# Performance work log

Hardware: AMD Instinct MI355X
Metric: run time of the kernel (lower is better)

Reference implementation:

```python
import jax, jax.numpy as jnp
import numpy as np

LOCAL_REGION = 16
GRANULARITY = 2048
INIT_RATIO = 8
EXPAND_RATIO = 2
C = 128
N_LAYERS = 5


def setup_inputs() -> dict:
    key = jax.random.key(0)
    ks = jax.random.split(key, 20)
    g = lambda k, s: jax.random.normal(k, s, dtype=jnp.float32) * 0.05
    z = lambda n: jnp.zeros((n,), jnp.float32)
    return {
        "batch_x": jax.random.normal(ks[0], (1, 16384, 4), dtype=jnp.float32),
        # PT: attr embedding (in_channel=1 -> 128), positional MLP (3->128->128)
        "attr_w": g(ks[1], (1, C)), "attr_b": z(C),
        "pos_w1": g(ks[2], (3, C)), "pos_b1": z(C),
        "pos_w2": g(ks[3], (C, C)), "pos_b2": z(C),
        # 5 self-attention layers over the K-neighborhood
        "wq": g(ks[4], (N_LAYERS, C, C)),
        "wk": g(ks[5], (N_LAYERS, C, C)),
        "wv": g(ks[6], (N_LAYERS, C, C)),
        "wout": g(ks[7], (C, C)), "bout": z(C),
        # mu/sigma head: 128 -> 64 -> 16 -> 2
        "ms_w1": g(ks[8], (C, 64)), "ms_b1": z(64),
        "ms_w2": g(ks[9], (64, 16)), "ms_b2": z(16),
        "ms_w3": g(ks[10], (16, 2)), "ms_b3": z(2),
    }


def _window_schedule(N):
    base = min(N // INIT_RATIO, GRANULARITY)
    win = base
    sched = []
    cursor = base
    while cursor < N:
        win = min(win * EXPAND_RATIO, GRANULARITY)
        sched.append((cursor, min(win, N - cursor)))
        cursor += win
    return sched


def _forward(batch_x, attr_w, attr_b, pos_w1, pos_b1, pos_w2, pos_b2,
             wq, wk, wv, wout, bout, ms_w1, ms_b1, ms_w2, ms_b2, ms_w3, ms_b3):
    B, N, _ = batch_x.shape
    total_bits = jnp.float32(0.0)
    for cur, w in _window_schedule(N):
        context = batch_x[:, :cur, :]
        target = batch_x[:, cur:cur + w, :]
        tg, ta = target[..., :3], target[..., 3:]    # [B,M,3], [B,M,1]
        cg, ca = context[..., :3], context[..., 3:]  # [B,Nc,3], [B,Nc,1]
        # knn_points: brute-force squared distances, K smallest
        d2 = (jnp.sum(tg * tg, -1)[:, :, None] + jnp.sum(cg * cg, -1)[:, None, :]
              - 2.0 * jnp.einsum('bmd,bnd->bmn', tg, cg))  # [B,M,Nc]
        _, idx = jax.lax.top_k(-d2, LOCAL_REGION)            # [B,M,K]
        # knn_gather
        gg = jnp.take_along_axis(cg[:, None], idx[..., None], axis=2)  # [B,M,K,3]
        ga = jnp.take_along_axis(ca[:, None], idx[..., None], axis=2)  # [B,M,K,1]
        # n_scale_ball: center each neighborhood, scale into unit ball
        gg = gg - jnp.mean(gg, axis=2, keepdims=True)
        r = jnp.max(jnp.linalg.norm(gg, axis=-1, keepdims=True), axis=2, keepdims=True)
        gg = gg / jnp.maximum(r, 1e-8)
        # PT: pos-encoded grouped self-attention, max-pool over K
        pos = jax.nn.relu(gg @ pos_w1 + pos_b1) @ pos_w2 + pos_b2  # [B,M,K,C]
        f = ga @ attr_w + attr_b + pos
        for l in range(N_LAYERS):
            q, k, v = f @ wq[l], f @ wk[l], f @ wv[l]
            a = jax.nn.softmax(jnp.einsum('bmkc,bmjc->bmkj', q, k)
                               / jnp.sqrt(jnp.float32(C)), axis=-1)
            f = f + jnp.einsum('bmkj,bmjc->bmkc', a, v)
        feat = jnp.max(f @ wout + bout, axis=2)  # [B,M,C]
        # mu/sigma head
        h = jax.nn.relu(feat @ ms_w1 + ms_b1)
        h = jax.nn.relu(h @ ms_w2 + ms_b2)
        ms = h @ ms_w3 + ms_b3
        mu, sigma = ms[..., :1], jnp.exp(ms[..., 1:])
        # feature_probs_based_mu_sigma: bits under quantized Gaussian
        inv = 1.0 / (sigma * jnp.sqrt(jnp.float32(2.0)))
        probs = 0.5 * (jax.lax.erf((ta + 0.5 - mu) * inv)
                       - jax.lax.erf((ta - 0.5 - mu) * inv))
        total_bits = total_bits + jnp.sum(jnp.clip(-jnp.log2(probs + 1e-10), 0.0, 50.0))
    return total_bits


def reference(batch_x, attr_w, attr_b, pos_w1, pos_b1, pos_w2, pos_b2,
              wq, wk, wv, wout, bout, ms_w1, ms_b1, ms_w2, ms_b2, ms_w3, ms_b3):
    return _forward(batch_x, attr_w, attr_b, pos_w1, pos_b1, pos_w2, pos_b2,
                    wq, wk, wv, wout, bout, ms_w1, ms_b1, ms_w2, ms_b2, ms_w3, ms_b3)
```

## Files before the change

kernel.cpp:

```cpp
#include <hip/hip_runtime.h>
#include <math.h>

#define NPTS 16384
#define WWIN 2048
#define NWIN 7
#define KNB  16
#define CDIM 128
#define NTGT (NPTS - WWIN)
#define TPB  4
#define NBLK (NTGT / TPB)
#define NMAT 12

typedef _Float16 f16;
typedef __attribute__((ext_vector_type(8))) _Float16 f16x8;
typedef __attribute__((ext_vector_type(4))) _Float16 f16x4;
typedef __attribute__((ext_vector_type(2))) _Float16 f16x2;
typedef __attribute__((ext_vector_type(4))) float f32x4;

#define MFMA16(a, b, c) __builtin_amdgcn_mfma_f32_16x16x32_f16((a), (b), (c), 0, 0, 0)

__device__ __forceinline__ unsigned umax_(unsigned a, unsigned b) { return a > b ? a : b; }
__device__ __forceinline__ unsigned umin_(unsigned a, unsigned b) { return a < b ? a : b; }

__global__ void prep_kernel(const float* __restrict__ pos_w2,
                            const float* __restrict__ wq,
                            const float* __restrict__ wk,
                            const float* __restrict__ wv,
                            const float* __restrict__ wout,
                            f16* __restrict__ wt) {
  const int i = blockIdx.x * 256 + threadIdx.x;
  if (i >= NMAT * 16384) return;
  const int mat = i >> 14;
  const int e   = i & 16383;
  const int k   = e >> 7;
  const int n   = e & 127;
  if (mat < 7) {
    const float* src = (mat == 0) ? pos_w2 : (mat <= 5 ? wv + (mat - 1) * 16384 : wout);
    wt[mat * 16384 + n * 128 + k] = (f16)src[k * 128 + n];
  } else {
    const int l = mat - 7;
    const float* qr = wq + l * 16384 + k * 128;
    const float* kr = wk + l * 16384 + n * 128;
    float sacc = 0.f;
#pragma unroll 4
    for (int c = 0; c < 128; ++c) sacc += qr[c] * kr[c];
    wt[mat * 16384 + n * 128 + k] = (f16)sacc;
  }
}

__device__ __forceinline__ f16x8 ldA(const f16* __restrict__ buf, int l15, int lg,
                                     int mt, int kc) {
  const int row = mt * 16 + l15;
  const int col = (kc * 32 + lg * 8) ^ ((row & 7) << 3);
  return *(const f16x8*)(buf + row * 128 + col);
}

__device__ __forceinline__ void stD(f16* __restrict__ buf, int l15, int lg, int n0,
                                    int mt, int nt, const f32x4 v) {
#pragma unroll
  for (int r = 0; r < 4; ++r) {
    const int row = mt * 16 + lg * 4 + r;
    const int col = (n0 + nt * 16 + l15) ^ ((row & 7) << 3);
    buf[row * 128 + col] = (f16)v[r];
  }
}

__device__ __forceinline__ void zacc(f32x4 (&acc)[4][2]) {
#pragma unroll
  for (int mt = 0; mt < 4; ++mt)
#pragma unroll
    for (int nt = 0; nt < 2; ++nt) acc[mt][nt] = (f32x4){0.f, 0.f, 0.f, 0.f};
}

__device__ __forceinline__ void gemm_tile(const f16* __restrict__ src,
                                          const f16* __restrict__ wmat,
                                          int l15, int lg, int n0,
                                          f32x4 (&acc)[4][2]) {
#pragma unroll
  for (int kc = 0; kc < 4; ++kc) {
    const f16x8 b0 = *(const f16x8*)(wmat + (n0 + l15) * 128 + kc * 32 + lg * 8);
    const f16x8 b1 = *(const f16x8*)(wmat + (n0 + 16 + l15) * 128 + kc * 32 + lg * 8);
#pragma unroll
    for (int mt = 0; mt < 4; ++mt) {
      const f16x8 a = ldA(src, l15, lg, mt, kc);
      acc[mt][0] = MFMA16(a, b0, acc[mt][0]);
      acc[mt][1] = MFMA16(a, b1, acc[mt][1]);
    }
  }
}

__global__ __launch_bounds__(256, 2)
void nn_kernel(
    const float4* __restrict__ bx, const f16* __restrict__ wt,
    const float* __restrict__ attr_w, const float* __restrict__ attr_b,
    const float* __restrict__ pos_w1, const float* __restrict__ pos_b1,
    const float* __restrict__ pos_b2, const float* __restrict__ bout,
    const float* __restrict__ ms_w1, const float* __restrict__ ms_b1,
    const float* __restrict__ ms_w2, const float* __restrict__ ms_b2,
    const float* __restrict__ ms_w3, const float* __restrict__ ms_b3,
    float* __restrict__ partials) {
  __shared__ __align__(16) f16 fA[64 * 128];
  __shared__ __align__(16) f16 qA[64 * 128];
  __shared__ __align__(16) f16 vtB[128 * 64];
  __shared__ __align__(16) f16 pA[TPB * 512];

  const int t     = threadIdx.x;
  const int wv    = t >> 6;
  const int lane  = t & 63;
  const int l15   = lane & 15;
  const int lg    = lane >> 4;
  const int n0    = wv * 32;
  const int slot0 = (NBLK - 1 - blockIdx.x) * TPB;

  {
    const int  slot = slot0 + wv;
    const int  cur  = WWIN * ((slot0 >> 11) + 1);
    const float4 tp = bx[WWIN + slot];

    unsigned u0 = 0xFFFFFFF0u, u1 = 0xFFFFFFF1u, u2 = 0xFFFFFFF2u, u3 = 0xFFFFFFF3u;

#define INS4(P) { const unsigned p_ = (P);                                     \
    const unsigned t0 = umax_(u0, p_); u0 = umin_(u0, p_);                     \
    const unsigned t1 = umax_(u1, t0); u1 = umin_(u1, t0);                     \
    const unsigned t2 = umax_(u2, t1); u2 = umin_(u2, t1);                     \
    u3 = umin_(u3, t2); }

    float4 ca = bx[lane];
    float4 cb = bx[lane + 64];
    for (int j = lane; j < cur; j += 128) {
      const float4 na = bx[j + 128];
      const float4 nb = bx[j + 192];
      const float dx0 = tp.x - ca.x, dy0 = tp.y - ca.y, dz0 = tp.z - ca.z;
      const float dx1 = tp.x - cb.x, dy1 = tp.y - cb.y, dz1 = tp.z - cb.z;
      const float d20 = dx0 * dx0 + dy0 * dy0 + dz0 * dz0;
      const float d21 = dx1 * dx1 + dy1 * dy1 + dz1 * dz1;
      const unsigned p0 = ((__float_as_uint(d20) << 1) & 0xFFFFC000u) | (unsigned)j;
      const unsigned p1 = ((__float_as_uint(d21) << 1) & 0xFFFFC000u) | (unsigned)(j + 64);
      INS4(p0)
      INS4(p1)
      ca = na; cb = nb;
    }
#undef INS4

    unsigned* nbr = ((unsigned*)pA) + 960;
    for (int n = 0; n < 16; ++n) {
      unsigned m = u0;
      m = umin_(m, (unsigned)__shfl_xor((int)m, 1));
      m = umin_(m, (unsigned)__shfl_xor((int)m, 2));
      m = umin_(m, (unsigned)__shfl_xor((int)m, 4));
      m = umin_(m, (unsigned)__shfl_xor((int)m, 8));
      m = umin_(m, (unsigned)__shfl_xor((int)m, 16));
      m = umin_(m, (unsigned)__shfl_xor((int)m, 32));
      if (lane == n) nbr[wv * 16 + n] = m & 0x3FFFu;
      if (u0 == m) {
        u0 = u1; u1 = u2; u2 = u3; u3 = 0xFFFFFFFFu;
      }
    }
  }
  __syncthreads();

  float* ggs = (float*)pA;
  if (t < 64) {
    const int nid  = (int)(((unsigned*)pA)[960 + t]);
    const float4 p = bx[nid];
    float sx = p.x, sy = p.y, sz = p.z;
#pragma unroll
    for (int m = 1; m < 16; m <<= 1) {
      sx += __shfl_xor(sx, m); sy += __shfl_xor(sy, m); sz += __shfl_xor(sz, m);
    }
    const float gx = p.x - sx * 0.0625f;
    const float gy = p.y - sy * 0.0625f;
    const float gz = p.z - sz * 0.0625f;
    float nr = sqrtf(gx * gx + gy * gy + gz * gz);
#pragma unroll
    for (int m = 1; m < 16; m <<= 1) nr = fmaxf(nr, __shfl_xor(nr, m));
    const float inv = 1.f / fmaxf(nr, 1e-8f);
    ggs[t * 4 + 0] = gx * inv; ggs[t * 4 + 1] = gy * inv;
    ggs[t * 4 + 2] = gz * inv; ggs[t * 4 + 3] = p.w;
  }
  __syncthreads();

  {
    const int row = t & 63;
    const int cb  = (t >> 6) * 32;
    const float gx = ggs[row * 4], gy = ggs[row * 4 + 1], gz = ggs[row * 4 + 2];
#pragma unroll
    for (int c = cb; c < cb + 32; c += 2) {
      const float h0 = pos_b1[c]     + gx * pos_w1[c]     + gy * pos_w1[128 + c]     + gz * pos_w1[256 + c];
      const float h1 = pos_b1[c + 1] + gx * pos_w1[c + 1] + gy * pos_w1[128 + c + 1] + gz * pos_w1[256 + c + 1];
      f16x2 pr; pr[0] = (f16)fmaxf(h0, 0.f); pr[1] = (f16)fmaxf(h1, 0.f);
      *(f16x2*)(qA + row * 128 + (c ^ ((row & 7) << 3))) = pr;
    }
  }
  __syncthreads();

  f32x4 facc[4][2];
  {
    zacc(facc);
    gemm_tile(qA, wt, l15, lg, n0, facc);
#pragma unroll
    for (int nt = 0; nt < 2; ++nt) {
      const int col = n0 + nt * 16 + l15;
      const float bias = pos_b2[col] + attr_b[col];
      const float aw   = attr_w[col];
#pragma unroll
      for (int mt = 0; mt < 4; ++mt) {
#pragma unroll
        for (int r = 0; r < 4; ++r)
          facc[mt][nt][r] += bias + ggs[(mt * 16 + lg * 4 + r) * 4 + 3] * aw;
        stD(fA, l15, lg, n0, mt, nt, facc[mt][nt]);
      }
    }
  }
  __syncthreads();

  *(f16x8*)(pA + t * 8) = (f16x8){0, 0, 0, 0, 0, 0, 0, 0};

  for (int l = 0; l < 5; ++l) {
    {
      f32x4 acc[4][2];
      zacc(acc);
      gemm_tile(fA, wt + (7 + l) * 16384, l15, lg, n0, acc);
#pragma unroll
      for (int mt = 0; mt < 4; ++mt)
#pragma unroll
        for (int nt = 0; nt < 2; ++nt) stD(qA, l15, lg, n0, mt, nt, acc[mt][nt]);
      zacc(acc);
      gemm_tile(fA, wt + (1 + l) * 16384, l15, lg, n0, acc);
#pragma unroll
      for (int mt = 0; mt < 4; ++mt)
#pragma unroll
        for (int nt = 0; nt < 2; ++nt) {
          const int ch = n0 + nt * 16 + l15;
          const int r0 = (mt * 16 + lg * 4) ^ ((ch & 7) << 3);
          f16x4 p;
#pragma unroll
          for (int r = 0; r < 4; ++r) p[r] = (f16)acc[mt][nt][r];
          *(f16x4*)(vtB + ch * 64 + r0) = p;
        }
    }
    __syncthreads();
    {
      f32x4 s = (f32x4){0.f, 0.f, 0.f, 0.f};
#pragma unroll
      for (int kc = 0; kc < 4; ++kc)
        s = MFMA16(ldA(qA, l15, lg, wv, kc), ldA(fA, l15, lg, wv, kc), s);
#pragma unroll
      for (int r = 0; r < 4; ++r) {
        float v = s[r] * 0.08838834764831844055f;
        float mx = v;
#pragma unroll
        for (int m = 1; m < 16; m <<= 1) mx = fmaxf(mx, __shfl_xor(mx, m));
        const float e = __expf(v - mx);
        float sm = e;
#pragma unroll
        for (int m = 1; m < 16; m <<= 1) sm += __shfl_xor(sm, m);
        pA[wv * 512 + (lg * 4 + r) * 32 + l15] = (f16)(e / sm);
      }
    }
    __syncthreads();
    {
#pragma unroll
      for (int tt = 0; tt < 4; ++tt) {
        const f16x8 a = *(const f16x8*)(pA + tt * 512 + l15 * 32 + lg * 8);
#pragma unroll
        for (int nt = 0; nt < 2; ++nt) {
          const int colb = n0 + nt * 16 + l15;
          const int r0 = (tt * 16 + 8 * (lg & 1)) ^ ((colb & 7) << 3);
          const f16x8 b = *(const f16x8*)(vtB + colb * 64 + r0);
          facc[tt][nt] = MFMA16(a, b, facc[tt][nt]);
          stD(fA, l15, lg, n0, tt, nt, facc[tt][nt]);
        }
      }
    }
    __syncthreads();
  }

  float* feats = (float*)pA;
  float* h1s   = feats + 512;
  float* h2s   = h1s + 256;
  float* btmp  = h2s + 64;
  {
    f32x4 acc[4][2];
    zacc(acc);
    gemm_tile(fA, wt + 6 * 16384, l15, lg, n0, acc);
#pragma unroll
    for (int nt = 0; nt < 2; ++nt) {
      const int col = n0 + nt * 16 + l15;
      const float bo = bout[col];
#pragma unroll
      for (int mt = 0; mt < 4; ++mt) {
        const f32x4 v = acc[mt][nt];
        float m = fmaxf(fmaxf(v[0], v[1]), fmaxf(v[2], v[3])) + bo;
        m = fmaxf(m, __shfl_xor(m, 16));
        m = fmaxf(m, __shfl_xor(m, 32));
        if (lg == 0) feats[mt * 128 + col] = m;
      }
    }
  }
  __syncthreads();
  {
    const int tt = t >> 6, h = t & 63;
    float a = ms_b1[h];
#pragma unroll 4
    for (int c = 0; c < 128; ++c) a += feats[tt * 128 + c] * ms_w1[c * 64 + h];
    h1s[tt * 64 + h] = fmaxf(a, 0.f);
  }
  __syncthreads();
  if (t < 64) {
    const int tt = t >> 4, h = t & 15;
    float a = ms_b2[h];
#pragma unroll 4
    for (int c = 0; c < 64; ++c) a += h1s[tt * 64 + c] * ms_w2[c * 16 + h];
    h2s[tt * 16 + h] = fmaxf(a, 0.f);
  }
  __syncthreads();
  if (t < TPB) {
    float mu = ms_b3[0], lgs = ms_b3[1];
#pragma unroll
    for (int c = 0; c < 16; ++c) {
      mu  += h2s[t * 16 + c] * ms_w3[2 * c];
      lgs += h2s[t * 16 + c] * ms_w3[2 * c + 1];
    }
    const float sigma = expf(lgs);
    const float inv   = 1.f / (sigma * 1.41421356237309504880f);
    const float ta    = ((const float*)bx)[(WWIN + slot0 + t) * 4 + 3];
    const float p = 0.5f * (erff((ta + 0.5f - mu) * inv) - erff((ta - 0.5f - mu) * inv));
    float bits = -log2f(p + 1e-10f);
    btmp[t] = fminf(fmaxf(bits, 0.f), 50.f);
  }
  __syncthreads();
  if (t == 0) partials[blockIdx.x] = btmp[0] + btmp[1] + btmp[2] + btmp[3];
}

__global__ void reduce_kernel(const float* __restrict__ partials, float* __restrict__ out) {
  float s = 0.f;
  for (int i = threadIdx.x; i < NBLK; i += 256) s += partials[i];
#pragma unroll
  for (int m = 1; m < 64; m <<= 1) s += __shfl_xor(s, m);
  __shared__ float wsum[4];
  if ((threadIdx.x & 63) == 0) wsum[threadIdx.x >> 6] = s;
  __syncthreads();
  if (threadIdx.x == 0) out[0] = wsum[0] + wsum[1] + wsum[2] + wsum[3];
}

extern "C" void kernel_launch(void* const* d_in, const int* in_sizes, int n_in,
                              void* d_out, int out_size, void* d_ws, size_t ws_size,
                              hipStream_t stream) {
  const float4* bx     = (const float4*)d_in[0];
  const float* attr_w  = (const float*)d_in[1];
  const float* attr_b  = (const float*)d_in[2];
  const float* pos_w1  = (const float*)d_in[3];
  const float* pos_b1  = (const float*)d_in[4];
  const float* pos_w2  = (const float*)d_in[5];
  const float* pos_b2  = (const float*)d_in[6];
  const float* wq      = (const float*)d_in[7];
  const float* wk      = (const float*)d_in[8];
  const float* wv      = (const float*)d_in[9];
  const float* wout    = (const float*)d_in[10];
  const float* bout    = (const float*)d_in[11];
  const float* ms_w1   = (const float*)d_in[12];
  const float* ms_b1   = (const float*)d_in[13];
  const float* ms_w2   = (const float*)d_in[14];
  const float* ms_b2   = (const float*)d_in[15];
  const float* ms_w3   = (const float*)d_in[16];
  const float* ms_b3   = (const float*)d_in[17];

  f16*   wt       = (f16*)((char*)d_ws);
  float* partials = (float*)((char*)d_ws + (1u << 19));

  prep_kernel<<<(NMAT * 16384 + 255) / 256, 256, 0, stream>>>(pos_w2, wq, wk, wv, wout, wt);
  nn_kernel<<<NBLK, 256, 0, stream>>>(bx, wt, attr_w, attr_b,
                                      pos_w1, pos_b1, pos_b2, bout,
                                      ms_w1, ms_b1, ms_w2, ms_b2, ms_w3, ms_b3,
                                      partials);
  reduce_kernel<<<1, 256, 0, stream>>>(partials, (float*)d_out);
}
```

Baseline: 386.6 us.

## Process eight targets per block with 512 threads and reuse qA for V

Each block now handles 8 target points instead of 4, using 8 waves arranged as two row groups times four column groups. The GEMM helpers take a row offset so each wave covers its 64-row slice of a 128-row tile, and weight B-fragments are shared across more rows. The separate vtB buffer is dropped: V is computed after the softmax and written transposed into qA, which costs an extra barrier. Block count is halved and LDS per block roughly doubles, which may limit occupancy.

```diff
diff --git a/kernel.cpp b/kernel.cpp
--- a/kernel.cpp
+++ b/kernel.cpp
@@ -7,7 +7,7 @@
 #define KNB  16
 #define CDIM 128
 #define NTGT (NPTS - WWIN)
-#define TPB  4
+#define TPB  8
 #define NBLK (NTGT / TPB)
 #define NMAT 12
 
@@ -48,19 +48,19 @@
   }
 }
 
-__device__ __forceinline__ f16x8 ldA(const f16* __restrict__ buf, int l15, int lg,
-                                     int mt, int kc) {
-  const int row = mt * 16 + l15;
+__device__ __forceinline__ f16x8 ldA(const f16* __restrict__ buf, int row0,
+                                     int l15, int lg, int kc) {
+  const int row = row0 + l15;
   const int col = (kc * 32 + lg * 8) ^ ((row & 7) << 3);
   return *(const f16x8*)(buf + row * 128 + col);
 }
 
-__device__ __forceinline__ void stD(f16* __restrict__ buf, int l15, int lg, int n0,
-                                    int mt, int nt, const f32x4 v) {
+__device__ __forceinline__ void stD(f16* __restrict__ buf, int row0, int col0,
+                                    int l15, int lg, const f32x4 v) {
 #pragma unroll
   for (int r = 0; r < 4; ++r) {
-    const int row = mt * 16 + lg * 4 + r;
-    const int col = (n0 + nt * 16 + l15) ^ ((row & 7) << 3);
+    const int row = row0 + lg * 4 + r;
+    const int col = (col0 + l15) ^ ((row & 7) << 3);
     buf[row * 128 + col] = (f16)v[r];
   }
 }
@@ -74,7 +74,7 @@
 
 __device__ __forceinline__ void gemm_tile(const f16* __restrict__ src,
                                           const f16* __restrict__ wmat,
-                                          int l15, int lg, int n0,
+                                          int l15, int lg, int mrow0, int n0,
                                           f32x4 (&acc)[4][2]) {
 #pragma unroll
   for (int kc = 0; kc < 4; ++kc) {
@@ -82,14 +82,14 @@
     const f16x8 b1 = *(const f16x8*)(wmat + (n0 + 16 + l15) * 128 + kc * 32 + lg * 8);
 #pragma unroll
     for (int mt = 0; mt < 4; ++mt) {
-      const f16x8 a = ldA(src, l15, lg, mt, kc);
+      const f16x8 a = ldA(src, mrow0 + mt * 16, l15, lg, kc);
       acc[mt][0] = MFMA16(a, b0, acc[mt][0]);
       acc[mt][1] = MFMA16(a, b1, acc[mt][1]);
     }
   }
 }
 
-__global__ __launch_bounds__(256, 2)
+__global__ __launch_bounds__(512, 2)
 void nn_kernel(
     const float4* __restrict__ bx, const f16* __restrict__ wt,
     const float* __restrict__ attr_w, const float* __restrict__ attr_b,
@@ -99,21 +99,23 @@
     const float* __restrict__ ms_w2, const float* __restrict__ ms_b2,
     const float* __restrict__ ms_w3, const float* __restrict__ ms_b3,
     float* __restrict__ partials) {
-  __shared__ __align__(16) f16 fA[64 * 128];
-  __shared__ __align__(16) f16 qA[64 * 128];
-  __shared__ __align__(16) f16 vtB[128 * 64];
+  __shared__ __align__(16) f16 fA[128 * 128];
+  __shared__ __align__(16) f16 qA[128 * 128];
   __shared__ __align__(16) f16 pA[TPB * 512];
 
   const int t     = threadIdx.x;
-  const int wv    = t >> 6;
+  const int wid   = t >> 6;
+  const int mg    = wid >> 2;
+  const int cg    = wid & 3;
   const int lane  = t & 63;
   const int l15   = lane & 15;
   const int lg    = lane >> 4;
-  const int n0    = wv * 32;
+  const int n0    = cg * 32;
+  const int mrow0 = mg * 64;
   const int slot0 = (NBLK - 1 - blockIdx.x) * TPB;
 
   {
-    const int  slot = slot0 + wv;
+    const int  slot = slot0 + wid;
     const int  cur  = WWIN * ((slot0 >> 11) + 1);
     const float4 tp = bx[WWIN + slot];
 
@@ -142,7 +144,7 @@
     }
 #undef INS4
 
-    unsigned* nbr = ((unsigned*)pA) + 960;
+    unsigned* nbr = ((unsigned*)pA) + 1920;
     for (int n = 0; n < 16; ++n) {
       unsigned m = u0;
       m = umin_(m, (unsigned)__shfl_xor((int)m, 1));
@@ -151,7 +153,7 @@
       m = umin_(m, (unsigned)__shfl_xor((int)m, 8));
       m = umin_(m, (unsigned)__shfl_xor((int)m, 16));
       m = umin_(m, (unsigned)__shfl_xor((int)m, 32));
-      if (lane == n) nbr[wv * 16 + n] = m & 0x3FFFu;
+      if (lane == n) nbr[wid * 16 + n] = m & 0x3FFFu;
       if (u0 == m) {
         u0 = u1; u1 = u2; u2 = u3; u3 = 0xFFFFFFFFu;
       }
@@ -160,8 +162,8 @@
   __syncthreads();
 
   float* ggs = (float*)pA;
-  if (t < 64) {
-    const int nid  = (int)(((unsigned*)pA)[960 + t]);
+  if (t < 128) {
+    const int nid  = (int)(((unsigned*)pA)[1920 + t]);
     const float4 p = bx[nid];
     float sx = p.x, sy = p.y, sz = p.z;
 #pragma unroll
@@ -181,8 +183,8 @@
   __syncthreads();
 
   {
-    const int row = t & 63;
-    const int cb  = (t >> 6) * 32;
+    const int row = t & 127;
+    const int cb  = (t >> 7) * 32;
     const float gx = ggs[row * 4], gy = ggs[row * 4 + 1], gz = ggs[row * 4 + 2];
 #pragma unroll
     for (int c = cb; c < cb + 32; c += 2) {
@@ -197,7 +199,7 @@
   f32x4 facc[4][2];
   {
     zacc(facc);
-    gemm_tile(qA, wt, l15, lg, n0, facc);
+    gemm_tile(qA, wt, l15, lg, mrow0, n0, facc);
 #pragma unroll
     for (int nt = 0; nt < 2; ++nt) {
       const int col = n0 + nt * 16 + l15;
@@ -207,8 +209,8 @@
       for (int mt = 0; mt < 4; ++mt) {
 #pragma unroll
         for (int r = 0; r < 4; ++r)
-          facc[mt][nt][r] += bias + ggs[(mt * 16 + lg * 4 + r) * 4 + 3] * aw;
-        stD(fA, l15, lg, n0, mt, nt, facc[mt][nt]);
+          facc[mt][nt][r] += bias + ggs[(mrow0 + mt * 16 + lg * 4 + r) * 4 + 3] * aw;
+        stD(fA, mrow0 + mt * 16, n0 + nt * 16, l15, lg, facc[mt][nt]);
       }
     }
   }
@@ -220,31 +222,19 @@
     {
       f32x4 acc[4][2];
       zacc(acc);
-      gemm_tile(fA, wt + (7 + l) * 16384, l15, lg, n0, acc);
+      gemm_tile(fA, wt + (7 + l) * 16384, l15, lg, mrow0, n0, acc);
 #pragma unroll
       for (int mt = 0; mt < 4; ++mt)
 #pragma unroll
-        for (int nt = 0; nt < 2; ++nt) stD(qA, l15, lg, n0, mt, nt, acc[mt][nt]);
-      zacc(acc);
-      gemm_tile(fA, wt + (1 + l) * 16384, l15, lg, n0, acc);
-#pragma unroll
-      for (int mt = 0; mt < 4; ++mt)
-#pragma unroll
-        for (int nt = 0; nt < 2; ++nt) {
-          const int ch = n0 + nt * 16 + l15;
-          const int r0 = (mt * 16 + lg * 4) ^ ((ch & 7) << 3);
-          f16x4 p;
-#pragma unroll
-          for (int r = 0; r < 4; ++r) p[r] = (f16)acc[mt][nt][r];
-          *(f16x4*)(vtB + ch * 64 + r0) = p;
-        }
+        for (int nt = 0; nt < 2; ++nt)
+          stD(qA, mrow0 + mt * 16, n0 + nt * 16, l15, lg, acc[mt][nt]);
     }
     __syncthreads();
     {
       f32x4 s = (f32x4){0.f, 0.f, 0.f, 0.f};
 #pragma unroll
       for (int kc = 0; kc < 4; ++kc)
-        s = MFMA16(ldA(qA, l15, lg, wv, kc), ldA(fA, l15, lg, wv, kc), s);
+        s = MFMA16(ldA(qA, wid * 16, l15, lg, kc), ldA(fA, wid * 16, l15, lg, kc), s);
 #pragma unroll
       for (int r = 0; r < 4; ++r) {
         float v = s[r] * 0.08838834764831844055f;
@@ -255,21 +245,40 @@
         float sm = e;
 #pragma unroll
         for (int m = 1; m < 16; m <<= 1) sm += __shfl_xor(sm, m);
-        pA[wv * 512 + (lg * 4 + r) * 32 + l15] = (f16)(e / sm);
+        pA[wid * 512 + (lg * 4 + r) * 32 + l15] = (f16)(e / sm);
       }
     }
     __syncthreads();
     {
+      f32x4 acc[4][2];
+      zacc(acc);
+      gemm_tile(fA, wt + (1 + l) * 16384, l15, lg, mrow0, n0, acc);
+      __syncthreads();
+#pragma unroll
+      for (int mt = 0; mt < 4; ++mt)
+#pragma unroll
+        for (int nt = 0; nt < 2; ++nt) {
+          const int ch = n0 + nt * 16 + l15;
+          const int r0 = (mrow0 + mt * 16 + lg * 4) ^ ((ch & 7) << 3);
+          f16x4 p;
+#pragma unroll
+          for (int r = 0; r < 4; ++r) p[r] = (f16)acc[mt][nt][r];
+          *(f16x4*)(qA + ch * 128 + r0) = p;
+        }
+    }
+    __syncthreads();
+    {
 #pragma unroll
       for (int tt = 0; tt < 4; ++tt) {
-        const f16x8 a = *(const f16x8*)(pA + tt * 512 + l15 * 32 + lg * 8);
+        const int gt = mg * 4 + tt;
+        const f16x8 a = *(const f16x8*)(pA + gt * 512 + l15 * 32 + lg * 8);
 #pragma unroll
         for (int nt = 0; nt < 2; ++nt) {
           const int colb = n0 + nt * 16 + l15;
-          const int r0 = (tt * 16 + 8 * (lg & 1)) ^ ((colb & 7) << 3);
-          const f16x8 b = *(const f16x8*)(vtB + colb * 64 + r0);
+          const int r0 = (gt * 16 + 8 * (lg & 1)) ^ ((colb & 7) << 3);
+          const f16x8 b = *(const f16x8*)(qA + colb * 128 + r0);
           facc[tt][nt] = MFMA16(a, b, facc[tt][nt]);
-          stD(fA, l15, lg, n0, tt, nt, facc[tt][nt]);
+          stD(fA, gt * 16, n0 + nt * 16, l15, lg, facc[tt][nt]);
         }
       }
     }
@@ -277,13 +286,13 @@
   }
 
   float* feats = (float*)pA;
-  float* h1s   = feats + 512;
-  float* h2s   = h1s + 256;
-  float* btmp  = h2s + 64;
+  float* h1s   = feats + 1024;
+  float* h2s   = h1s + 512;
+  float* btmp  = h2s + 128;
   {
     f32x4 acc[4][2];
     zacc(acc);
-    gemm_tile(fA, wt + 6 * 16384, l15, lg, n0, acc);
+    gemm_tile(fA, wt + 6 * 16384, l15, lg, mrow0, n0, acc);
 #pragma unroll
     for (int nt = 0; nt < 2; ++nt) {
       const int col = n0 + nt * 16 + l15;
@@ -294,7 +303,7 @@
         float m = fmaxf(fmaxf(v[0], v[1]), fmaxf(v[2], v[3])) + bo;
         m = fmaxf(m, __shfl_xor(m, 16));
         m = fmaxf(m, __shfl_xor(m, 32));
-        if (lg == 0) feats[mt * 128 + col] = m;
+        if (lg == 0) feats[(mg * 4 + mt) * 128 + col] = m;
       }
     }
   }
@@ -307,7 +316,7 @@
     h1s[tt * 64 + h] = fmaxf(a, 0.f);
   }
   __syncthreads();
-  if (t < 64) {
+  if (t < 128) {
     const int tt = t >> 4, h = t & 15;
     float a = ms_b2[h];
 #pragma unroll 4
@@ -330,7 +339,12 @@
     btmp[t] = fminf(fmaxf(bits, 0.f), 50.f);
   }
   __syncthreads();
-  if (t == 0) partials[blockIdx.x] = btmp[0] + btmp[1] + btmp[2] + btmp[3];
+  if (t == 0) {
+    float s = 0.f;
+#pragma unroll
+    for (int q = 0; q < TPB; ++q) s += btmp[q];
+    partials[blockIdx.x] = s;
+  }
 }
 
 __global__ void reduce_kernel(const float* __restrict__ partials, float* __restrict__ out) {
@@ -370,7 +384,7 @@
   float* partials = (float*)((char*)d_ws + (1u << 19));
 
   prep_kernel<<<(NMAT * 16384 + 255) / 256, 256, 0, stream>>>(pos_w2, wq, wk, wv, wout, wt);
-  nn_kernel<<<NBLK, 256, 0, stream>>>(bx, wt, attr_w, attr_b,
+  nn_kernel<<<NBLK, 512, 0, stream>>>(bx, wt, attr_w, attr_b,
                                       pos_w1, pos_b1, pos_b2, bout,
                                       ms_w1, ms_b1, ms_w2, ms_b2, ms_w3, ms_b3,
                                       partials);
```

Measured after the change: 450.7 us. 16.6% more time.

## Fuse attention PV into softmax per wave, unroll kNN scan with deeper prefetch

Applied to the files above, without the earlier changes.

Each wave now owns its own 16-row target tile for the residual update. It computes the PV product over all 128 channels right after its softmax, which removes one block-wide barrier per attention layer. The residual accumulator is reloaded from shared fp16 after the embedding, so the residual stream changes from fp32 registers to an fp16 round-trip at that point. The kNN distance scan is unrolled four times with eight outstanding prefetch loads to hide global latency. These add register pressure, and the loop now prefetches further past cur, which is still within the buffer.

```diff
diff --git a/kernel.cpp b/kernel.cpp
--- a/kernel.cpp
+++ b/kernel.cpp
@@ -48,19 +48,19 @@
   }
 }
 
-__device__ __forceinline__ f16x8 ldA(const f16* __restrict__ buf, int l15, int lg,
-                                     int mt, int kc) {
-  const int row = mt * 16 + l15;
+__device__ __forceinline__ f16x8 ldA(const f16* __restrict__ buf, int row0,
+                                     int l15, int lg, int kc) {
+  const int row = row0 + l15;
   const int col = (kc * 32 + lg * 8) ^ ((row & 7) << 3);
   return *(const f16x8*)(buf + row * 128 + col);
 }
 
-__device__ __forceinline__ void stD(f16* __restrict__ buf, int l15, int lg, int n0,
-                                    int mt, int nt, const f32x4 v) {
+__device__ __forceinline__ void stD(f16* __restrict__ buf, int row0, int col0,
+                                    int l15, int lg, const f32x4 v) {
 #pragma unroll
   for (int r = 0; r < 4; ++r) {
-    const int row = mt * 16 + lg * 4 + r;
-    const int col = (n0 + nt * 16 + l15) ^ ((row & 7) << 3);
+    const int row = row0 + lg * 4 + r;
+    const int col = (col0 + l15) ^ ((row & 7) << 3);
     buf[row * 128 + col] = (f16)v[r];
   }
 }
@@ -82,7 +82,7 @@
     const f16x8 b1 = *(const f16x8*)(wmat + (n0 + 16 + l15) * 128 + kc * 32 + lg * 8);
 #pragma unroll
     for (int mt = 0; mt < 4; ++mt) {
-      const f16x8 a = ldA(src, l15, lg, mt, kc);
+      const f16x8 a = ldA(src, mt * 16, l15, lg, kc);
       acc[mt][0] = MFMA16(a, b0, acc[mt][0]);
       acc[mt][1] = MFMA16(a, b1, acc[mt][1]);
     }
@@ -102,7 +102,7 @@
   __shared__ __align__(16) f16 fA[64 * 128];
   __shared__ __align__(16) f16 qA[64 * 128];
   __shared__ __align__(16) f16 vtB[128 * 64];
-  __shared__ __align__(16) f16 pA[TPB * 512];
+  __shared__ __align__(16) char aux[4096];
 
   const int t     = threadIdx.x;
   const int wv    = t >> 6;
@@ -112,6 +112,10 @@
   const int n0    = wv * 32;
   const int slot0 = (NBLK - 1 - blockIdx.x) * TPB;
 
+  f16* pA = (f16*)aux;
+  unsigned* nbr = (unsigned*)aux;
+  float* ggs = (float*)(aux + 1024);
+
   {
     const int  slot = slot0 + wv;
     const int  cur  = WWIN * ((slot0 >> 11) + 1);
@@ -124,25 +128,32 @@
     const unsigned t1 = umax_(u1, t0); u1 = umin_(u1, t0);                     \
     const unsigned t2 = umax_(u2, t1); u2 = umin_(u2, t1);                     \
     u3 = umin_(u3, t2); }
-
-    float4 ca = bx[lane];
-    float4 cb = bx[lane + 64];
-    for (int j = lane; j < cur; j += 128) {
-      const float4 na = bx[j + 128];
-      const float4 nb = bx[j + 192];
-      const float dx0 = tp.x - ca.x, dy0 = tp.y - ca.y, dz0 = tp.z - ca.z;
-      const float dx1 = tp.x - cb.x, dy1 = tp.y - cb.y, dz1 = tp.z - cb.z;
-      const float d20 = dx0 * dx0 + dy0 * dy0 + dz0 * dz0;
-      const float d21 = dx1 * dx1 + dy1 * dy1 + dz1 * dz1;
-      const unsigned p0 = ((__float_as_uint(d20) << 1) & 0xFFFFC000u) | (unsigned)j;
-      const unsigned p1 = ((__float_as_uint(d21) << 1) & 0xFFFFC000u) | (unsigned)(j + 64);
-      INS4(p0)
-      INS4(p1)
-      ca = na; cb = nb;
-    }
+#define PROC(CA, CB, JJ) {                                                     \
+    const float dx0 = tp.x - (CA).x, dy0 = tp.y - (CA).y, dz0 = tp.z - (CA).z; \
+    const float dx1 = tp.x - (CB).x, dy1 = tp.y - (CB).y, dz1 = tp.z - (CB).z; \
+    const float d20 = dx0 * dx0 + dy0 * dy0 + dz0 * dz0;                       \
+    const float d21 = dx1 * dx1 + dy1 * dy1 + dz1 * dz1;                       \
+    const unsigned p0 = ((__float_as_uint(d20) << 1) & 0xFFFFC000u) | (unsigned)(JJ);      \
+    const unsigned p1 = ((__float_as_uint(d21) << 1) & 0xFFFFC000u) | (unsigned)((JJ) + 64); \
+    INS4(p0) INS4(p1) }
+
+    float4 a0 = bx[lane],       b0 = bx[lane + 64];
+    float4 a1 = bx[lane + 128], b1 = bx[lane + 192];
+    float4 a2 = bx[lane + 256], b2 = bx[lane + 320];
+    float4 a3 = bx[lane + 384], b3 = bx[lane + 448];
+    for (int j = lane; j < cur; j += 512) {
+      const float4 n0_ = bx[j + 512], n1_ = bx[j + 576];
+      const float4 n2_ = bx[j + 640], n3_ = bx[j + 704];
+      const float4 n4_ = bx[j + 768], n5_ = bx[j + 832];
+      const float4 n6_ = bx[j + 896], n7_ = bx[j + 960];
+      PROC(a0, b0, j)       a0 = n0_; b0 = n1_;
+      PROC(a1, b1, j + 128) a1 = n2_; b1 = n3_;
+      PROC(a2, b2, j + 256) a2 = n4_; b2 = n5_;
+      PROC(a3, b3, j + 384) a3 = n6_; b3 = n7_;
+    }
+#undef PROC
 #undef INS4
 
-    unsigned* nbr = ((unsigned*)pA) + 960;
     for (int n = 0; n < 16; ++n) {
       unsigned m = u0;
       m = umin_(m, (unsigned)__shfl_xor((int)m, 1));
@@ -152,16 +163,13 @@
       m = umin_(m, (unsigned)__shfl_xor((int)m, 16));
       m = umin_(m, (unsigned)__shfl_xor((int)m, 32));
       if (lane == n) nbr[wv * 16 + n] = m & 0x3FFFu;
-      if (u0 == m) {
-        u0 = u1; u1 = u2; u2 = u3; u3 = 0xFFFFFFFFu;
-      }
-    }
-  }
-  __syncthreads();
-
-  float* ggs = (float*)pA;
+      if (u0 == m) { u0 = u1; u1 = u2; u2 = u3; u3 = 0xFFFFFFFFu; }
+    }
+  }
+  __syncthreads();
+
   if (t < 64) {
-    const int nid  = (int)(((unsigned*)pA)[960 + t]);
+    const int nid  = (int)nbr[t];
     const float4 p = bx[nid];
     float sx = p.x, sy = p.y, sz = p.z;
 #pragma unroll
@@ -194,10 +202,10 @@
   }
   __syncthreads();
 
-  f32x4 facc[4][2];
-  {
-    zacc(facc);
-    gemm_tile(qA, wt, l15, lg, n0, facc);
+  {
+    f32x4 acc[4][2];
+    zacc(acc);
+    gemm_tile(qA, wt, l15, lg, n0, acc);
 #pragma unroll
     for (int nt = 0; nt < 2; ++nt) {
       const int col = n0 + nt * 16 + l15;
@@ -205,15 +213,26 @@
       const float aw   = attr_w[col];
 #pragma unroll
       for (int mt = 0; mt < 4; ++mt) {
+        f32x4 v = acc[mt][nt];
 #pragma unroll
         for (int r = 0; r < 4; ++r)
-          facc[mt][nt][r] += bias + ggs[(mt * 16 + lg * 4 + r) * 4 + 3] * aw;
-        stD(fA, l15, lg, n0, mt, nt, facc[mt][nt]);
+          v[r] += bias + ggs[(mt * 16 + lg * 4 + r) * 4 + 3] * aw;
+        stD(fA, mt * 16, n0 + nt * 16, l15, lg, v);
       }
     }
   }
   __syncthreads();
 
+  f32x4 facc8[8];
+#pragma unroll
+  for (int nt = 0; nt < 8; ++nt) {
+    const int col = nt * 16 + l15;
+#pragma unroll
+    for (int r = 0; r < 4; ++r) {
+      const int row = wv * 16 + lg * 4 + r;
+      facc8[nt][r] = (float)fA[row * 128 + (col ^ ((row & 7) << 3))];
+    }
+  }
   *(f16x8*)(pA + t * 8) = (f16x8){0, 0, 0, 0, 0, 0, 0, 0};
 
   for (int l = 0; l < 5; ++l) {
@@ -224,7 +243,8 @@
 #pragma unroll
       for (int mt = 0; mt < 4; ++mt)
 #pragma unroll
-        for (int nt = 0; nt < 2; ++nt) stD(qA, l15, lg, n0, mt, nt, acc[mt][nt]);
+        for (int nt = 0; nt < 2; ++nt)
+          stD(qA, mt * 16, n0 + nt * 16, l15, lg, acc[mt][nt]);
       zacc(acc);
       gemm_tile(fA, wt + (1 + l) * 16384, l15, lg, n0, acc);
 #pragma unroll
@@ -244,7 +264,7 @@
       f32x4 s = (f32x4){0.f, 0.f, 0.f, 0.f};
 #pragma unroll
       for (int kc = 0; kc < 4; ++kc)
-        s = MFMA16(ldA(qA, l15, lg, wv, kc), ldA(fA, l15, lg, wv, kc), s);
+        s = MFMA16(ldA(qA, wv * 16, l15, lg, kc), ldA(fA, wv * 16, l15, lg, kc), s);
 #pragma unroll
       for (int r = 0; r < 4; ++r) {
         float v = s[r] * 0.08838834764831844055f;
@@ -257,26 +277,20 @@
         for (int m = 1; m < 16; m <<= 1) sm += __shfl_xor(sm, m);
         pA[wv * 512 + (lg * 4 + r) * 32 + l15] = (f16)(e / sm);
       }
+      const f16x8 a = *(const f16x8*)(pA + wv * 512 + l15 * 32 + lg * 8);
+#pragma unroll
+      for (int nt = 0; nt < 8; ++nt) {
+        const int ch = nt * 16 + l15;
+        const int r0 = (wv * 16 + 8 * (lg & 1)) ^ ((ch & 7) << 3);
+        const f16x8 b = *(const f16x8*)(vtB + ch * 64 + r0);
+        facc8[nt] = MFMA16(a, b, facc8[nt]);
+        stD(fA, wv * 16, nt * 16, l15, lg, facc8[nt]);
+      }
     }
     __syncthreads();
-    {
-#pragma unroll
-      for (int tt = 0; tt < 4; ++tt) {
-        const f16x8 a = *(const f16x8*)(pA + tt * 512 + l15 * 32 + lg * 8);
-#pragma unroll
-        for (int nt = 0; nt < 2; ++nt) {
-          const int colb = n0 + nt * 16 + l15;
-          const int r0 = (tt * 16 + 8 * (lg & 1)) ^ ((colb & 7) << 3);
-          const f16x8 b = *(const f16x8*)(vtB + colb * 64 + r0);
-          facc[tt][nt] = MFMA16(a, b, facc[tt][nt]);
-          stD(fA, l15, lg, n0, tt, nt, facc[tt][nt]);
-        }
-      }
-    }
-    __syncthreads();
-  }
-
-  float* feats = (float*)pA;
+  }
+
+  float* feats = (float*)aux;
   float* h1s   = feats + 512;
   float* h2s   = h1s + 256;
   float* btmp  = h2s + 64;
```

Result: faster. 365.0 us (-5.6%).
